# Performance work log

Measured on AMD Instinct MI355X. Metric: run time of the kernel, lower is better.

Reference implementation:

```python
import jax, jax.numpy as jnp
import numpy as np

B, S, D, H, HD = 2, 2048, 1024, 16, 64
K, L = 1024, 4  # num_codes, vq_levels


def setup_inputs() -> dict:
    key = jax.random.key(0)
    ks = jax.random.split(key, 12)
    w = lambda k, shape: jax.random.normal(k, shape, jnp.float32) * 0.02
    return {
        "x": jax.random.normal(ks[0], (B, S, D), jnp.float32),
        "ln1_g": jnp.ones((D,), jnp.float32), "ln1_b": jnp.zeros((D,), jnp.float32),
        "wq": w(ks[1], (D, D)), "wk": w(ks[2], (D, D)), "wv": w(ks[3], (D, D)),
        "wg": w(ks[4], (D, D)), "wo": w(ks[5], (D, D)),
        "ln2_g": jnp.ones((D,), jnp.float32), "ln2_b": jnp.zeros((D,), jnp.float32),
        "w1": w(ks[6], (D, 4 * D)), "b1": jnp.zeros((4 * D,), jnp.float32),
        "w2": w(ks[7], (4 * D, D)), "b2": jnp.zeros((D,), jnp.float32),
        "ln3_g": jnp.ones((D,), jnp.float32), "ln3_b": jnp.zeros((D,), jnp.float32),
        "codebooks": jax.random.uniform(ks[8], (L, K, D), jnp.float32, -1.0 / K, 1.0 / K),
    }


def _ln(x, g, b):
    m = jnp.mean(x, -1, keepdims=True)
    v = jnp.var(x, -1, keepdims=True)
    return (x - m) / jnp.sqrt(v + 1e-5) * g + b


def _rope(x):  # x: [B, S, H, HD]
    hd = x.shape[-1]
    inv = 1.0 / (10000.0 ** (jnp.arange(0, hd, 2, dtype=jnp.float32) / hd))
    t = jnp.arange(x.shape[1], dtype=jnp.float32)
    f = jnp.einsum('i,j->ij', t, inv)               # [S, HD/2]
    emb = jnp.concatenate([f, f], -1)               # [S, HD]
    cos = jnp.cos(emb)[None, :, None, :]
    sin = jnp.sin(emb)[None, :, None, :]
    x1, x2 = jnp.split(x, 2, -1)
    rot = jnp.concatenate([-x2, x1], -1)
    return x * cos + rot * sin


def reference(x, ln1_g, ln1_b, wq, wk, wv, wg, wo, ln2_g, ln2_b,
              w1, b1, w2, b2, ln3_g, ln3_b, codebooks):
    # --- retention sub-block (pre-LN) ---
    h = _ln(x, ln1_g, ln1_b)
    q = (h @ wq).reshape(B, S, H, HD)
    k = (h @ wk).reshape(B, S, H, HD)
    v = (h @ wv).reshape(B, S, H, HD)
    q, k = _rope(q), _rope(k)
    q, k, v = (a.transpose(0, 2, 1, 3) for a in (q, k, v))  # [B,H,S,HD]
    i = jnp.arange(S)
    dmask = jnp.tril(i[:, None] - i[None, :]).astype(jnp.float32)  # [S,S], >=0
    gamma = (1.0 - jnp.exp2(-5.0 - jnp.arange(H, dtype=jnp.float32)))[:, None, None]
    decay = (gamma ** dmask) * jnp.tril(jnp.ones((S, S), jnp.float32))  # [H,S,S]
    ret = jnp.einsum('bhqd,bhkd->bhqk', q, k) / np.sqrt(HD).astype(np.float32) * decay
    o = jnp.einsum('bhqk,bhkd->bhqd', ret, v).transpose(0, 2, 1, 3).reshape(B, S, D)
    g = jax.nn.silu(h @ wg)
    x = x + (o * g) @ wo
    # --- MLP sub-block (pre-LN) ---
    h2 = _ln(x, ln2_g, ln2_b)
    x = x + (jax.nn.gelu(h2 @ w1 + b1, approximate=False) @ w2 + b2)
    # --- residual vector quantizer ---
    xn = _ln(x, ln3_g, ln3_b)
    residual, total = xn, jnp.zeros_like(xn)
    ql, el = 0.0, 0.0
    for lvl in range(L):
        cb = codebooks[lvl]                         # [K, D]
        flat = residual.reshape(-1, D)              # [B*S, D]
        d2 = (jnp.sum(flat ** 2, 1, keepdims=True)
              + jnp.sum(cb ** 2, 1) - 2.0 * flat @ cb.T)
        idx = jnp.argmin(d2, 1)
        quant = cb[idx].reshape(xn.shape)
        ql = ql + jnp.mean((quant - jax.lax.stop_gradient(residual)) ** 2)
        el = el + jnp.mean((jax.lax.stop_gradient(quant) - residual) ** 2)
        total = total + quant
        residual = residual - jax.lax.stop_gradient(quant)
    final = xn + jax.lax.stop_gradient(total - xn)  # straight-through
    return (x + final, ql / L, el / L)
```

## Files before the change

kernel.cpp:

```cpp
#include <hip/hip_runtime.h>
#include <cstdint>
#include <cstddef>

#define DEV __device__ __forceinline__

typedef __attribute__((ext_vector_type(8))) short bf16x8;
typedef __attribute__((ext_vector_type(4))) float f32x4;

typedef const __attribute__((address_space(1))) void gl_void;
typedef __attribute__((address_space(3))) void lds_void;

DEV unsigned short f2bf(float f){
  union { float f; uint32_t u; } v; v.f = f;
  uint32_t r = v.u + 0x7FFFu + ((v.u >> 16) & 1u);
  return (unsigned short)(r >> 16);
}
DEV float bf2f(unsigned short u){
  union { uint32_t u; float f; } v; v.u = ((uint32_t)u) << 16; return v.f;
}
DEV uint32_t packbf2(float a, float b){
  return (uint32_t)f2bf(a) | ((uint32_t)f2bf(b) << 16);
}

__global__ void ln_kernel(const float* __restrict__ x, const float* __restrict__ gw,
                          const float* __restrict__ bw, unsigned short* __restrict__ obf,
                          float* __restrict__ of32)
{
  const int row = blockIdx.x, t = threadIdx.x;
  const float4 v = ((const float4*)(x + (size_t)row*1024))[t];
  float s  = v.x + v.y + v.z + v.w;
  float s2 = v.x*v.x + v.y*v.y + v.z*v.z + v.w*v.w;
  #pragma unroll
  for (int o = 32; o >= 1; o >>= 1){ s += __shfl_down(s, o); s2 += __shfl_down(s2, o); }
  __shared__ float red[8];
  const int w = t >> 6, ln = t & 63;
  if (ln == 0){ red[w] = s; red[4+w] = s2; }
  __syncthreads();
  const float fs  = red[0]+red[1]+red[2]+red[3];
  const float fs2 = red[4]+red[5]+red[6]+red[7];
  const float mean = fs * (1.0f/1024.0f);
  const float var  = fs2 * (1.0f/1024.0f) - mean*mean;
  const float rstd = rsqrtf(var + 1e-5f);
  const float4 gv = ((const float4*)gw)[t];
  const float4 bv = ((const float4*)bw)[t];
  float4 o4;
  o4.x = (v.x-mean)*rstd*gv.x + bv.x;
  o4.y = (v.y-mean)*rstd*gv.y + bv.y;
  o4.z = (v.z-mean)*rstd*gv.z + bv.z;
  o4.w = (v.w-mean)*rstd*gv.w + bv.w;
  if (of32) ((float4*)(of32 + (size_t)row*1024))[t] = o4;
  ushort4 ob; ob.x = f2bf(o4.x); ob.y = f2bf(o4.y); ob.z = f2bf(o4.z); ob.w = f2bf(o4.w);
  ((ushort4*)(obf + (size_t)row*1024))[t] = ob;
}

struct Ptr5 { const float* p[5]; };
__global__ void transpose_cvt5(Ptr5 in, unsigned short* __restrict__ out)
{
  __shared__ float tile[32][33];
  const float* src = in.p[blockIdx.z];
  unsigned short* dst = out + (size_t)blockIdx.z*1048576;
  const int c0 = blockIdx.x*32, r0 = blockIdx.y*32;
  const int tx = threadIdx.x & 31, ty = threadIdx.x >> 5;
  #pragma unroll
  for (int i = 0; i < 32; i += 8)
    tile[ty+i][tx] = src[(size_t)(r0+ty+i)*1024 + c0 + tx];
  __syncthreads();
  #pragma unroll
  for (int i = 0; i < 32; i += 8)
    dst[(size_t)(c0+ty+i)*1024 + r0 + tx] = f2bf(tile[tx][ty+i]);
}

__global__ void transpose_cvt(const float* __restrict__ in, unsigned short* __restrict__ out,
                              int R, int C)
{
  __shared__ float tile[32][33];
  const int c0 = blockIdx.x*32, r0 = blockIdx.y*32;
  const int tx = threadIdx.x & 31, ty = threadIdx.x >> 5;
  #pragma unroll
  for (int i = 0; i < 32; i += 8)
    tile[ty+i][tx] = in[(size_t)(r0+ty+i)*C + c0 + tx];
  __syncthreads();
  #pragma unroll
  for (int i = 0; i < 32; i += 8)
    out[(size_t)(c0+ty+i)*R + r0 + tx] = f2bf(tile[tx][ty+i]);
}

__global__ void cvt_bf16x4(const float* __restrict__ in, unsigned short* __restrict__ out)
{
  const int i = blockIdx.x*256 + threadIdx.x;
  const float4 v = ((const float4*)in)[i];
  ushort4 o; o.x = f2bf(v.x); o.y = f2bf(v.y); o.z = f2bf(v.z); o.w = f2bf(v.w);
  ((ushort4*)out)[i] = o;
}

__global__ void cbn2_kernel(const float* __restrict__ cb, float* __restrict__ cbn2)
{
  const int w = threadIdx.x >> 6, ln = threadIdx.x & 63;
  const int code = blockIdx.x*4 + w;
  const float4* cr = (const float4*)(cb + (size_t)code*1024);
  float s = 0.f;
  for (int i = ln; i < 256; i += 64){ float4 v = cr[i]; s += v.x*v.x+v.y*v.y+v.z*v.z+v.w*v.w; }
  #pragma unroll
  for (int o = 32; o >= 1; o >>= 1) s += __shfl_down(s, o);
  if (ln == 0) cbn2[code] = s;
}

__global__ void rope_kernel(unsigned short* __restrict__ q, unsigned short* __restrict__ k)
{
  const int tid = blockIdx.x*256 + threadIdx.x;
  const int j  = tid & 31;
  const int hh = (tid >> 5) & 15;
  const int s_ = (tid >> 9) & 2047;
  const int b  = tid >> 20;
  const float inv = exp2f(-(float)j * 0.4152410118609203f);
  const float f = (float)s_ * inv;
  float sn, cs; sincosf(f, &sn, &cs);
  const size_t base = ((size_t)(b*2048 + s_))*1024 + hh*64 + j;
  {
    float x1 = bf2f(q[base]), x2 = bf2f(q[base+32]);
    q[base]    = f2bf(x1*cs - x2*sn);
    q[base+32] = f2bf(x2*cs + x1*sn);
  }
  {
    float x1 = bf2f(k[base]), x2 = bf2f(k[base+32]);
    k[base]    = f2bf(x1*cs - x2*sn);
    k[base+32] = f2bf(x2*cs + x1*sn);
  }
}

template<int EPI, bool BIAS, bool RES, bool OUTBF>
__global__ __launch_bounds__(256, 2) void gemm_bt(
    const unsigned short* __restrict__ A, const unsigned short* __restrict__ BT,
    void* __restrict__ Cv, const float* __restrict__ bias, const float* __restrict__ resid,
    int M, int N, int K)
{
  __shared__ __align__(16) unsigned short As[2][128*64];
  __shared__ __align__(16) unsigned short Bs[2][128*64];
  const int t = threadIdx.x;
  const int w = t >> 6, ln = t & 63, lg = ln >> 4, lc = ln & 15;
  const int gx = gridDim.x, nwg = gridDim.x * gridDim.y;
  int lin = blockIdx.y * gx + blockIdx.x;
  lin = (lin >> 3) + (lin & 7) * (nwg >> 3);
  const int m0 = (lin / gx) * 128, n0 = (lin % gx) * 128;
  const int wr = (w >> 1) * 64, wc = (w & 1) * 64;
  f32x4 acc[4][4] = {};
  const int nkt = K >> 6;

  auto stage = [&](int buf, int kt){
    #pragma unroll
    for (int c = 0; c < 4; ++c){
      const int chunk = c*256 + t;
      const int row = chunk >> 3;
      const int kb = (((chunk & 7) << 4) ^ ((row & 7) << 4)) >> 1;
      __builtin_amdgcn_global_load_lds(
          (gl_void*)(A + (size_t)(m0+row)*K + (size_t)kt*64 + kb),
          (lds_void*)&As[buf][(c*256 + w*64)*8], 16, 0, 0);
      __builtin_amdgcn_global_load_lds(
          (gl_void*)(BT + (size_t)(n0+row)*K + (size_t)kt*64 + kb),
          (lds_void*)&Bs[buf][(c*256 + w*64)*8], 16, 0, 0);
    }
  };

  stage(0, 0);
  __syncthreads();
  for (int kt = 0; kt < nkt; ++kt){
    const int cur = kt & 1;
    if (kt + 1 < nkt) stage(cur ^ 1, kt + 1);
    #pragma unroll
    for (int ks = 0; ks < 2; ++ks){
      bf16x8 af[4], bfr[4];
      #pragma unroll
      for (int i = 0; i < 4; ++i){
        const int rowA = wr + i*16 + lc;
        const int rowB = wc + i*16 + lc;
        const int colA = (((ks<<6) + (lg<<4)) ^ ((rowA & 7) << 4)) >> 1;
        const int colB = (((ks<<6) + (lg<<4)) ^ ((rowB & 7) << 4)) >> 1;
        af[i]  = *(const bf16x8*)&As[cur][rowA*64 + colA];
        bfr[i] = *(const bf16x8*)&Bs[cur][rowB*64 + colB];
      }
      #pragma unroll
      for (int m = 0; m < 4; ++m)
        #pragma unroll
        for (int n = 0; n < 4; ++n)
          acc[m][n] = __builtin_amdgcn_mfma_f32_16x16x32_bf16(af[m], bfr[n], acc[m][n], 0, 0, 0);
    }
    __syncthreads();
  }

  #pragma unroll
  for (int m = 0; m < 4; ++m){
    #pragma unroll
    for (int n = 0; n < 4; ++n){
      #pragma unroll
      for (int r = 0; r < 4; ++r){
        const int row = m0 + wr + m*16 + lg*4 + r;
        const int col = n0 + wc + n*16 + lc;
        float v = acc[m][n][r];
        if constexpr (BIAS) v += bias[col];
        if constexpr (EPI == 1) v = v * (1.0f / (1.0f + __expf(-v)));
        if constexpr (EPI == 2) v = 0.5f * v * (1.0f + erff(v * 0.70710678118654752f));
        if constexpr (EPI == 3){
          const int sect = col >> 10;
          float ov = v;
          if (sect == 3) ov = v * (1.0f / (1.0f + __expf(-v)));
          ((unsigned short*)Cv)[(size_t)sect*4194304 + (size_t)row*1024 + (col & 1023)] = f2bf(ov);
          continue;
        }
        if constexpr (RES) v += resid[(size_t)row*N + col];
        if constexpr (OUTBF) ((unsigned short*)Cv)[(size_t)row*N + col] = f2bf(v);
        else                 ((float*)Cv)[(size_t)row*N + col] = v;
      }
    }
  }
}

template<int EPI, bool BIAS, bool RES, bool OUTBF, int NSPLIT>
__global__ __launch_bounds__(256, 3) void gemm64_bt(
    const unsigned short* __restrict__ A, const unsigned short* __restrict__ BT,
    void* __restrict__ Cv, const float* __restrict__ bias, const float* __restrict__ resid,
    int M, int N, int K)
{
  __shared__ __align__(16) unsigned short As[2][64*64];
  __shared__ __align__(16) unsigned short Bs[2][128*64];
  const int t = threadIdx.x;
  const int w = t >> 6, ln = t & 63, lg = ln >> 4, lc = ln & 15;
  const int gx = gridDim.x, nwg = gridDim.x * gridDim.y;
  int lin = blockIdx.y * gx + blockIdx.x;
  lin = (lin >> 3) + (lin & 7) * (nwg >> 3);
  const int bx = lin % gx, by = lin / gx;
  const int m0 = by * 64, n0 = bx * 128;
  const int wr = (w >> 1) * 32, wc = (w & 1) * 64;
  f32x4 acc[2][4] = {};
  const int nkt = (K >> 6) / NSPLIT;
  const int ktb = (NSPLIT > 1) ? blockIdx.z * nkt : 0;

  auto stage = [&](int buf, int kt){
    {
      const int chunk = t;
    }
    #pragma unroll
    for (int c = 0; c < 2; ++c){
      const int chunk = c*256 + t;
      const int row = chunk >> 3;
      const int kb = (((chunk & 7) << 4) ^ ((row & 7) << 4)) >> 1;
      __builtin_amdgcn_global_load_lds(
          (gl_void*)(A + (size_t)(m0+row)*K + (size_t)(ktb+kt)*64 + kb),
          (lds_void*)&As[buf][(c*256 + w*64)*8], 16, 0, 0);
    }
    #pragma unroll
    for (int c = 0; c < 4; ++c){
      const int chunk = c*256 + t;
      const int row = chunk >> 3;
      const int kb = (((chunk & 7) << 4) ^ ((row & 7) << 4)) >> 1;
      __builtin_amdgcn_global_load_lds(
          (gl_void*)(BT + (size_t)(n0+row)*K + (size_t)(ktb+kt)*64 + kb),
          (lds_void*)&Bs[buf][(c*256 + w*64)*8], 16, 0, 0);
    }
  };

  stage(0, 0);
  __syncthreads();
  for (int kt = 0; kt < nkt; ++kt){
    const int cur = kt & 1;
    if (kt + 1 < nkt) stage(cur ^ 1, kt + 1);
    #pragma unroll
    for (int ks = 0; ks < 2; ++ks){
      bf16x8 af[2], bfr[4];
      #pragma unroll
      for (int i = 0; i < 2; ++i){
        const int rowA = wr + i*16 + lc;
        const int colA = (((ks<<6) + (lg<<4)) ^ ((rowA & 7) << 4)) >> 1;
        af[i] = *(const bf16x8*)&As[cur][rowA*64 + colA];
      }
      #pragma unroll
      for (int i = 0; i < 4; ++i){
        const int rowB = wc + i*16 + lc;
        const int colB = (((ks<<6) + (lg<<4)) ^ ((rowB & 7) << 4)) >> 1;
        bfr[i] = *(const bf16x8*)&Bs[cur][rowB*64 + colB];
      }
      #pragma unroll
      for (int m = 0; m < 2; ++m)
        #pragma unroll
        for (int n = 0; n < 4; ++n)
          acc[m][n] = __builtin_amdgcn_mfma_f32_16x16x32_bf16(af[m], bfr[n], acc[m][n], 0, 0, 0);
    }
    __syncthreads();
  }

  if constexpr (EPI == 4){
    #pragma unroll
    for (int m = 0; m < 2; ++m){
      #pragma unroll
      for (int r = 0; r < 4; ++r){
        float best = 3.4e38f; int bi = 0;
        #pragma unroll
        for (int n = 0; n < 4; ++n){
          const int col = n0 + wc + n*16 + lc;
          const float d = bias[col] - 2.0f*acc[m][n][r];
          if (d < best){ best = d; bi = col; }
        }
        #pragma unroll
        for (int o = 1; o < 16; o <<= 1){
          const float ob = __shfl_xor(best, o);
          const int oi = __shfl_xor(bi, o);
          if (ob < best || (ob == best && oi < bi)){ best = ob; bi = oi; }
        }
        if (lc == 0){
          const int row = m0 + wr + m*16 + lg*4 + r;
          ((float2*)Cv)[row*16 + bx*2 + (w & 1)] = make_float2(best, (float)bi);
        }
      }
    }
    return;
  }

  float* Cp = (float*)Cv + (NSPLIT > 1 ? (size_t)blockIdx.z * (size_t)M * N : 0);
  #pragma unroll
  for (int m = 0; m < 2; ++m){
    #pragma unroll
    for (int n = 0; n < 4; ++n){
      #pragma unroll
      for (int r = 0; r < 4; ++r){
        const int row = m0 + wr + m*16 + lg*4 + r;
        const int col = n0 + wc + n*16 + lc;
        float v = acc[m][n][r];
        if constexpr (BIAS) v += bias[col];
        if constexpr (RES) v += resid[(size_t)row*N + col];
        if constexpr (OUTBF) ((unsigned short*)Cv)[(size_t)row*N + col] = f2bf(v);
        else                 Cp[(size_t)row*N + col] = v;
      }
    }
  }
}

__global__ void splitk_reduce(const float* __restrict__ p, const float* __restrict__ bias,
                              const float* __restrict__ resid, float* __restrict__ out)
{
  const int i = blockIdx.x*256 + threadIdx.x;
  const float4 a = ((const float4*)p)[i];
  const float4 b = ((const float4*)(p + 4194304))[i];
  const float4 rv = ((const float4*)resid)[i];
  const float4 bv = ((const float4*)bias)[i & 255];
  float4 o;
  o.x = a.x + b.x + rv.x + bv.x;
  o.y = a.y + b.y + rv.y + bv.y;
  o.z = a.z + b.z + rv.z + bv.z;
  o.w = a.w + b.w + rv.w + bv.w;
  ((float4*)out)[i] = o;
}

__global__ __launch_bounds__(256, 2) void chunk_sum(
    const unsigned short* __restrict__ kb, const unsigned short* __restrict__ vb,
    float* __restrict__ Tbuf)
{
  __shared__ unsigned short KT[64*72];
  __shared__ unsigned short VT[64*72];
  const int t = threadIdx.x, w = t >> 6, ln = t & 63, lg = ln >> 4, lc = ln & 15;
  const int blk = blockIdx.x;
  const int bh = blk >> 5, c = blk & 31;
  const int b = bh >> 4, hh = bh & 15;
  const float lg2g = log2f(1.0f - exp2f(-5.0f - (float)hh));
  #pragma unroll
  for (int ch = 0; ch < 2; ++ch){
    const int chunk = ch*256 + t;
    const int i = chunk >> 3, d0 = (chunk & 7)*8;
    const size_t gofs = ((size_t)(b*2048 + c*64 + i))*1024 + hh*64 + d0;
    const float wi = exp2f(lg2g * (float)(64 - i));
    union {uint4 u; unsigned short s[8];} kv, vv;
    kv.u = *(const uint4*)(kb + gofs);
    vv.u = *(const uint4*)(vb + gofs);
    #pragma unroll
    for (int j = 0; j < 8; ++j){
      KT[(d0+j)*72 + i] = f2bf(bf2f(kv.s[j]) * wi);
      VT[(d0+j)*72 + i] = vv.s[j];
    }
  }
  __syncthreads();
  f32x4 acc[4] = {};
  #pragma unroll
  for (int ks = 0; ks < 2; ++ks){
    const bf16x8 af = *(const bf16x8*)&KT[(w*16 + lc)*72 + ks*32 + lg*8];
    #pragma unroll
    for (int n = 0; n < 4; ++n){
      const bf16x8 bf = *(const bf16x8*)&VT[(n*16 + lc)*72 + ks*32 + lg*8];
      acc[n] = __builtin_amdgcn_mfma_f32_16x16x32_bf16(af, bf, acc[n], 0, 0, 0);
    }
  }
  float* out = Tbuf + (size_t)blk*4096;
  #pragma unroll
  for (int n = 0; n < 4; ++n)
    #pragma unroll
    for (int r = 0; r < 4; ++r)
      out[(w*16 + lg*4 + r)*64 + n*16 + lc] = acc[n][r];
}

__global__ void chunk_scan(const float* __restrict__ Tbuf, unsigned short* __restrict__ statesT)
{
  const int bh = blockIdx.x, t = threadIdx.x;
  const int hh = bh & 15;
  const float gamma = 1.0f - exp2f(-5.0f - (float)hh);
  const float g64 = exp2f(log2f(gamma) * 64.0f);
  float S[16];
  #pragma unroll
  for (int j = 0; j < 16; ++j) S[j] = 0.f;
  const int dv = t >> 2, d0 = (t & 3) * 16;
  for (int c = 0; c < 32; ++c){
    const size_t base = ((size_t)(bh*32 + c))*4096;
    union { unsigned short s[8]; uint4 u; } p0, p1;
    #pragma unroll
    for (int j = 0; j < 8; ++j){ p0.s[j] = f2bf(S[j]); p1.s[j] = f2bf(S[8+j]); }
    *(uint4*)(statesT + base + t*16)     = p0.u;
    *(uint4*)(statesT + base + t*16 + 8) = p1.u;
    #pragma unroll
    for (int j = 0; j < 16; ++j)
      S[j] = g64*S[j] + Tbuf[base + (size_t)(d0 + j)*64 + dv];
  }
}

__global__ __launch_bounds__(256, 2) void retention_chunk(
    const unsigned short* __restrict__ qb, const unsigned short* __restrict__ kb,
    const unsigned short* __restrict__ vb, const unsigned short* __restrict__ gb,
    const unsigned short* __restrict__ statesT, unsigned short* __restrict__ og)
{
  __shared__ unsigned short VT[64*72];
  __shared__ unsigned short Pw[64*72];
  const int t = threadIdx.x, w = t >> 6, ln = t & 63, lg = ln >> 4, lc = ln & 15;
  const int blk = blockIdx.x;
  const int bh = blk >> 5, c = blk & 31;
  const int b = bh >> 4, hh = bh & 15;
  const float lg2g = log2f(1.0f - exp2f(-5.0f - (float)hh));
  float gpr[4];
  #pragma unroll
  for (int r = 0; r < 4; ++r) gpr[r] = exp2f(-lg2g * (float)r);
  const size_t rowbase = (size_t)(b*2048 + c*64);

  #pragma unroll
  for (int ch = 0; ch < 2; ++ch){
    const int chunk = ch*256 + t;
    const int i = chunk >> 3, d0 = (chunk & 7)*8;
    union {uint4 u; unsigned short s[8];} vv;
    vv.u = *(const uint4*)(vb + (rowbase + i)*1024 + hh*64 + d0);
    #pragma unroll
    for (int j = 0; j < 8; ++j) VT[(d0+j)*72 + i] = vv.s[j];
  }

  bf16x8 Qf[2], Kf[4][2];
  #pragma unroll
  for (int ks = 0; ks < 2; ++ks){
    union {uint4 u; bf16x8 f;} cv;
    cv.u = *(const uint4*)(qb + (rowbase + w*16 + lc)*1024 + hh*64 + ks*32 + lg*8);
    Qf[ks] = cv.f;
    #pragma unroll
    for (int mt = 0; mt < 4; ++mt){
      union {uint4 u; bf16x8 f;} kv;
      kv.u = *(const uint4*)(kb + (rowbase + mt*16 + lc)*1024 + hh*64 + ks*32 + lg*8);
      Kf[mt][ks] = kv.f;
    }
  }

  f32x4 st[4] = {};
  #pragma unroll
  for (int ks = 0; ks < 2; ++ks)
    #pragma unroll
    for (int mt = 0; mt < 4; ++mt)
      st[mt] = __builtin_amdgcn_mfma_f32_16x16x32_bf16(Kf[mt][ks], Qf[ks], st[mt], 0, 0, 0);

  __syncthreads();

  #pragma unroll
  for (int mt = 0; mt < 4; ++mt){
    const int kp = mt*16 + lg*4;
    const int qrow = w*16 + lc;
    const int delta0 = qrow - kp;
    const float dec0 = exp2f(lg2g * (float)delta0) * 0.125f;
    float vals[4];
    #pragma unroll
    for (int r = 0; r < 4; ++r)
      vals[r] = (delta0 >= r) ? st[mt][r] * dec0 * gpr[r] : 0.0f;
    uint2 pk; pk.x = packbf2(vals[0], vals[1]); pk.y = packbf2(vals[2], vals[3]);
    *(uint2*)&Pw[qrow*72 + kp] = pk;
  }

  f32x4 acc[4] = {};
  const unsigned short* Sbase = statesT + (size_t)blk*4096;
  #pragma unroll
  for (int ks = 0; ks < 2; ++ks)
    #pragma unroll
    for (int n = 0; n < 4; ++n){
      union {uint4 u; bf16x8 f;} sv;
      sv.u = *(const uint4*)(Sbase + (n*16 + lc)*64 + ks*32 + lg*8);
      acc[n] = __builtin_amdgcn_mfma_f32_16x16x32_bf16(Qf[ks], sv.f, acc[n], 0, 0, 0);
    }
  #pragma unroll
  for (int n = 0; n < 4; ++n)
    #pragma unroll
    for (int r = 0; r < 4; ++r)
      acc[n][r] *= exp2f(lg2g * (float)(w*16 + lg*4 + r)) * 0.125f;

  #pragma unroll
  for (int ks = 0; ks < 2; ++ks){
    const bf16x8 Pf = *(const bf16x8*)&Pw[(w*16 + lc)*72 + ks*32 + lg*8];
    #pragma unroll
    for (int n = 0; n < 4; ++n){
      const bf16x8 Vf = *(const bf16x8*)&VT[(n*16 + lc)*72 + ks*32 + lg*8];
      acc[n] = __builtin_amdgcn_mfma_f32_16x16x32_bf16(Pf, Vf, acc[n], 0, 0, 0);
    }
  }

  #pragma unroll
  for (int n = 0; n < 4; ++n){
    #pragma unroll
    for (int r = 0; r < 4; ++r){
      const size_t row = rowbase + w*16 + lg*4 + r;
      const int col = hh*64 + n*16 + lc;
      const float gv = bf2f(gb[row*1024 + col]);
      og[row*1024 + col] = f2bf(acc[n][r] * gv);
    }
  }
}

__global__ void rvq_update2(const float* __restrict__ cb_l, const float2* __restrict__ partials,
                            float* __restrict__ res, unsigned short* __restrict__ resb,
                            float* __restrict__ total, float* __restrict__ qlpart, int lvl)
{
  const int m = blockIdx.x, t = threadIdx.x;
  __shared__ int sid;
  if (t == 0){
    float best = 3.4e38f; int bi = 0;
    #pragma unroll
    for (int p = 0; p < 16; ++p){
      const float2 pr = partials[m*16 + p];
      if (pr.x < best){ best = pr.x; bi = (int)pr.y; }
    }
    sid = bi;
  }
  __syncthreads();
  const int id = sid;
  const float4 qv = ((const float4*)(cb_l + (size_t)id*1024))[t];
  const float4 rv = ((const float4*)(res + (size_t)m*1024))[t];
  float4 nr; nr.x = rv.x - qv.x; nr.y = rv.y - qv.y; nr.z = rv.z - qv.z; nr.w = rv.w - qv.w;
  float4 tv;
  if (lvl == 0){ tv = qv; }
  else { tv = ((const float4*)(total + (size_t)m*1024))[t];
         tv.x += qv.x; tv.y += qv.y; tv.z += qv.z; tv.w += qv.w; }
  ((float4*)(total + (size_t)m*1024))[t] = tv;
  ((float4*)(res   + (size_t)m*1024))[t] = nr;
  ushort4 nb; nb.x = f2bf(nr.x); nb.y = f2bf(nr.y); nb.z = f2bf(nr.z); nb.w = f2bf(nr.w);
  ((ushort4*)(resb + (size_t)m*1024))[t] = nb;
  float s = nr.x*nr.x + nr.y*nr.y + nr.z*nr.z + nr.w*nr.w;
  #pragma unroll
  for (int o = 32; o >= 1; o >>= 1) s += __shfl_down(s, o);
  __shared__ float red[4];
  if ((t & 63) == 0) red[t >> 6] = s;
  __syncthreads();
  if (t == 0) qlpart[lvl*4096 + m] = red[0]+red[1]+red[2]+red[3];
}

__global__ void final_add(const float* __restrict__ x2, const float* __restrict__ total,
                          float* __restrict__ out)
{
  int i = blockIdx.x*256 + threadIdx.x;
  const float4* a = (const float4*)x2;
  const float4* b = (const float4*)total;
  float4* o = (float4*)out;
  for (; i < 4194304/4; i += gridDim.x*256){
    float4 va = a[i], vb = b[i];
    va.x += vb.x; va.y += vb.y; va.z += vb.z; va.w += vb.w;
    o[i] = va;
  }
}

__global__ void ql_final(const float* __restrict__ qlpart, float* __restrict__ outs)
{
  const int t = threadIdx.x;
  float s = 0.f;
  for (int i = t; i < 16384; i += 256) s += qlpart[i];
  #pragma unroll
  for (int o = 32; o >= 1; o >>= 1) s += __shfl_down(s, o);
  __shared__ float red[4];
  if ((t & 63) == 0) red[t >> 6] = s;
  __syncthreads();
  if (t == 0){
    const float q = (red[0]+red[1]+red[2]+red[3]) * (1.0f/4194304.0f) * 0.25f;
    outs[0] = q; outs[1] = q;
  }
}

extern "C" void kernel_launch(void* const* d_in, const int* in_sizes, int n_in,
                              void* d_out, int out_size, void* d_ws, size_t ws_size,
                              hipStream_t stream)
{
  const float* x     = (const float*)d_in[0];
  const float* ln1_g = (const float*)d_in[1];
  const float* ln1_b = (const float*)d_in[2];
  const float* wq    = (const float*)d_in[3];
  const float* wk    = (const float*)d_in[4];
  const float* wv    = (const float*)d_in[5];
  const float* wg    = (const float*)d_in[6];
  const float* wo    = (const float*)d_in[7];
  const float* ln2_g = (const float*)d_in[8];
  const float* ln2_b = (const float*)d_in[9];
  const float* w1    = (const float*)d_in[10];
  const float* b1    = (const float*)d_in[11];
  const float* w2    = (const float*)d_in[12];
  const float* b2    = (const float*)d_in[13];
  const float* ln3_g = (const float*)d_in[14];
  const float* ln3_b = (const float*)d_in[15];
  const float* cb    = (const float*)d_in[16];

  char* ws = (char*)d_ws;
  const size_t MB = 1024*1024;
  unsigned short* wqkvgT = (unsigned short*)(ws + 0*MB);
  unsigned short* woT  = (unsigned short*)(ws + 8*MB);
  unsigned short* w1T  = (unsigned short*)(ws + 10*MB);
  unsigned short* w2T  = (unsigned short*)(ws + 18*MB);
  unsigned short* cbbf = (unsigned short*)(ws + 26*MB);
  float* cbn2     = (float*)(ws + 34*MB);
  float* qlpart   = (float*)(ws + 34*MB + 16*1024);
  float2* partials= (float2*)(ws + 34*MB + 128*1024);
  unsigned short* hbf  = (unsigned short*)(ws + 35*MB);
  unsigned short* qbuf = (unsigned short*)(ws + 43*MB);
  unsigned short* kbuf = (unsigned short*)(ws + 51*MB);
  unsigned short* vbuf = (unsigned short*)(ws + 59*MB);
  unsigned short* gbuf = (unsigned short*)(ws + 67*MB);
  float* skbuf  = (float*)(ws + 43*MB);
  unsigned short* ogb  = (unsigned short*)(ws + 75*MB);
  float* x1     = (float*)(ws + 83*MB);
  unsigned short* h2   = (unsigned short*)(ws + 99*MB);
  unsigned short* a1   = (unsigned short*)(ws + 107*MB);
  float* x2     = (float*)(ws + 139*MB);
  float* Tbuf   = (float*)(ws + 139*MB);
  float* resf   = (float*)(ws + 155*MB);
  unsigned short* statesT = (unsigned short*)(ws + 155*MB);
  unsigned short* resb = (unsigned short*)(ws + 171*MB);
  float* totalb = (float*)(ws + 187*MB);

  float* outf = (float*)d_out;

  Ptr5 p5; p5.p[0]=wq; p5.p[1]=wk; p5.p[2]=wv; p5.p[3]=wg; p5.p[4]=wo;
  hipLaunchKernelGGL(transpose_cvt5, dim3(32,32,5), dim3(256), 0, stream, p5, wqkvgT);
  hipLaunchKernelGGL(transpose_cvt, dim3(128,32), dim3(256), 0, stream, w1, w1T, 1024, 4096);
  hipLaunchKernelGGL(transpose_cvt, dim3(32,128), dim3(256), 0, stream, w2, w2T, 4096, 1024);
  hipLaunchKernelGGL(cvt_bf16x4,    dim3(4096),   dim3(256), 0, stream, cb, cbbf);
  hipLaunchKernelGGL(cbn2_kernel,   dim3(1024),   dim3(256), 0, stream, cb, cbn2);

  hipLaunchKernelGGL(ln_kernel, dim3(4096), dim3(256), 0, stream, x, ln1_g, ln1_b, hbf, (float*)nullptr);
  hipLaunchKernelGGL((gemm_bt<3,false,false,true>), dim3(32,32), dim3(256), 0, stream,
                     hbf, wqkvgT, (void*)qbuf, (const float*)nullptr, (const float*)nullptr, 4096, 4096, 1024);
  hipLaunchKernelGGL(rope_kernel, dim3(8192), dim3(256), 0, stream, qbuf, kbuf);
  hipLaunchKernelGGL(chunk_sum,  dim3(1024), dim3(256), 0, stream, kbuf, vbuf, Tbuf);
  hipLaunchKernelGGL(chunk_scan, dim3(32),   dim3(256), 0, stream, Tbuf, statesT);
  hipLaunchKernelGGL(retention_chunk, dim3(1024), dim3(256), 0, stream,
                     qbuf, kbuf, vbuf, gbuf, statesT, ogb);
  hipLaunchKernelGGL((gemm64_bt<0,false,true,false,1>), dim3(8,64), dim3(256), 0, stream,
                     ogb, wqkvgT + 4194304, (void*)x1, (const float*)nullptr, x, 4096, 1024, 1024);

  hipLaunchKernelGGL(ln_kernel, dim3(4096), dim3(256), 0, stream, x1, ln2_g, ln2_b, h2, (float*)nullptr);
  hipLaunchKernelGGL((gemm_bt<2,true,false,true>), dim3(32,32), dim3(256), 0, stream,
                     h2, w1T, (void*)a1, b1, (const float*)nullptr, 4096, 4096, 1024);
  hipLaunchKernelGGL((gemm64_bt<0,false,false,false,2>), dim3(8,64,2), dim3(256), 0, stream,
                     a1, w2T, (void*)skbuf, (const float*)nullptr, (const float*)nullptr, 4096, 1024, 4096);
  hipLaunchKernelGGL(splitk_reduce, dim3(4096), dim3(256), 0, stream, skbuf, b2, x1, x2);

  hipLaunchKernelGGL(ln_kernel, dim3(4096), dim3(256), 0, stream, x2, ln3_g, ln3_b, resb, resf);
  for (int lvl = 0; lvl < 4; ++lvl){
    hipLaunchKernelGGL((gemm64_bt<4,false,false,false,1>), dim3(8,64), dim3(256), 0, stream,
                       resb, cbbf + (size_t)lvl*1048576, (void*)partials,
                       cbn2 + lvl*1024, (const float*)nullptr, 4096, 1024, 1024);
    hipLaunchKernelGGL(rvq_update2, dim3(4096), dim3(256), 0, stream,
                       cb + (size_t)lvl*1048576, partials, resf, resb,
                       totalb, qlpart, lvl);
  }

  hipLaunchKernelGGL(final_add, dim3(2048), dim3(256), 0, stream, x2, totalb, outf);
  hipLaunchKernelGGL(ql_final, dim3(1), dim3(256), 0, stream, qlpart, outf + 4194304);
}
```

Baseline: 443.6 us.

## Fuse RoPE into QKV GEMM epilogue, merge codebook prep, drop RVQ total buffer

RoPE now runs in the QKV/G GEMM epilogue, pairing accumulator tiles n and n^2, and the standalone rope kernel is removed. The codebook bf16 conversion and norm computation are merged into one kernel. The RVQ total accumulator is replaced by the identity total = xn - final residual, which removes per-level total reads and writes. gemm_bt is also retiled to a K-step of 32 with an unswizzled LDS layout and launch bounds raised to 4 waves per SIMD, trading possible LDS bank conflicts and more barriers for higher occupancy.

Measured after the change: 433.0 us. -2.4%, faster.

```diff
diff --git a/kernel.cpp b/kernel.cpp
--- a/kernel.cpp
+++ b/kernel.cpp
@@ -85,57 +85,30 @@
     out[(size_t)(c0+ty+i)*R + r0 + tx] = f2bf(tile[tx][ty+i]);
 }
 
-__global__ void cvt_bf16x4(const float* __restrict__ in, unsigned short* __restrict__ out)
-{
-  const int i = blockIdx.x*256 + threadIdx.x;
-  const float4 v = ((const float4*)in)[i];
+__global__ void cvtnorm_kernel(const float* __restrict__ cb, unsigned short* __restrict__ cbbf,
+                               float* __restrict__ cbn2)
+{
+  const int code = blockIdx.x, t = threadIdx.x;
+  const float4 v = ((const float4*)(cb + (size_t)code*1024))[t];
   ushort4 o; o.x = f2bf(v.x); o.y = f2bf(v.y); o.z = f2bf(v.z); o.w = f2bf(v.w);
-  ((ushort4*)out)[i] = o;
-}
-
-__global__ void cbn2_kernel(const float* __restrict__ cb, float* __restrict__ cbn2)
-{
-  const int w = threadIdx.x >> 6, ln = threadIdx.x & 63;
-  const int code = blockIdx.x*4 + w;
-  const float4* cr = (const float4*)(cb + (size_t)code*1024);
-  float s = 0.f;
-  for (int i = ln; i < 256; i += 64){ float4 v = cr[i]; s += v.x*v.x+v.y*v.y+v.z*v.z+v.w*v.w; }
-  #pragma unroll
-  for (int o = 32; o >= 1; o >>= 1) s += __shfl_down(s, o);
-  if (ln == 0) cbn2[code] = s;
-}
-
-__global__ void rope_kernel(unsigned short* __restrict__ q, unsigned short* __restrict__ k)
-{
-  const int tid = blockIdx.x*256 + threadIdx.x;
-  const int j  = tid & 31;
-  const int hh = (tid >> 5) & 15;
-  const int s_ = (tid >> 9) & 2047;
-  const int b  = tid >> 20;
-  const float inv = exp2f(-(float)j * 0.4152410118609203f);
-  const float f = (float)s_ * inv;
-  float sn, cs; sincosf(f, &sn, &cs);
-  const size_t base = ((size_t)(b*2048 + s_))*1024 + hh*64 + j;
-  {
-    float x1 = bf2f(q[base]), x2 = bf2f(q[base+32]);
-    q[base]    = f2bf(x1*cs - x2*sn);
-    q[base+32] = f2bf(x2*cs + x1*sn);
-  }
-  {
-    float x1 = bf2f(k[base]), x2 = bf2f(k[base+32]);
-    k[base]    = f2bf(x1*cs - x2*sn);
-    k[base+32] = f2bf(x2*cs + x1*sn);
-  }
+  ((ushort4*)(cbbf + (size_t)code*1024))[t] = o;
+  float s = v.x*v.x + v.y*v.y + v.z*v.z + v.w*v.w;
+  #pragma unroll
+  for (int off = 32; off >= 1; off >>= 1) s += __shfl_down(s, off);
+  __shared__ float red[4];
+  if ((t & 63) == 0) red[t >> 6] = s;
+  __syncthreads();
+  if (t == 0) cbn2[code] = red[0]+red[1]+red[2]+red[3];
 }
 
 template<int EPI, bool BIAS, bool RES, bool OUTBF>
-__global__ __launch_bounds__(256, 2) void gemm_bt(
+__global__ __launch_bounds__(256, 4) void gemm_bt(
     const unsigned short* __restrict__ A, const unsigned short* __restrict__ BT,
     void* __restrict__ Cv, const float* __restrict__ bias, const float* __restrict__ resid,
     int M, int N, int K)
 {
-  __shared__ __align__(16) unsigned short As[2][128*64];
-  __shared__ __align__(16) unsigned short Bs[2][128*64];
+  __shared__ __align__(16) unsigned short As[2][128*32];
+  __shared__ __align__(16) unsigned short Bs[2][128*32];
   const int t = threadIdx.x;
   const int w = t >> 6, ln = t & 63, lg = ln >> 4, lc = ln & 15;
   const int gx = gridDim.x, nwg = gridDim.x * gridDim.y;
@@ -144,19 +117,18 @@
   const int m0 = (lin / gx) * 128, n0 = (lin % gx) * 128;
   const int wr = (w >> 1) * 64, wc = (w & 1) * 64;
   f32x4 acc[4][4] = {};
-  const int nkt = K >> 6;
+  const int nkt = K >> 5;
 
   auto stage = [&](int buf, int kt){
     #pragma unroll
-    for (int c = 0; c < 4; ++c){
+    for (int c = 0; c < 2; ++c){
       const int chunk = c*256 + t;
-      const int row = chunk >> 3;
-      const int kb = (((chunk & 7) << 4) ^ ((row & 7) << 4)) >> 1;
+      const int row = chunk >> 2, ke = (chunk & 3) * 8;
       __builtin_amdgcn_global_load_lds(
-          (gl_void*)(A + (size_t)(m0+row)*K + (size_t)kt*64 + kb),
+          (gl_void*)(A + (size_t)(m0+row)*K + (size_t)kt*32 + ke),
           (lds_void*)&As[buf][(c*256 + w*64)*8], 16, 0, 0);
       __builtin_amdgcn_global_load_lds(
-          (gl_void*)(BT + (size_t)(n0+row)*K + (size_t)kt*64 + kb),
+          (gl_void*)(BT + (size_t)(n0+row)*K + (size_t)kt*32 + ke),
           (lds_void*)&Bs[buf][(c*256 + w*64)*8], 16, 0, 0);
     }
   };
@@ -166,25 +138,48 @@
   for (int kt = 0; kt < nkt; ++kt){
     const int cur = kt & 1;
     if (kt + 1 < nkt) stage(cur ^ 1, kt + 1);
-    #pragma unroll
-    for (int ks = 0; ks < 2; ++ks){
-      bf16x8 af[4], bfr[4];
-      #pragma unroll
-      for (int i = 0; i < 4; ++i){
-        const int rowA = wr + i*16 + lc;
-        const int rowB = wc + i*16 + lc;
-        const int colA = (((ks<<6) + (lg<<4)) ^ ((rowA & 7) << 4)) >> 1;
-        const int colB = (((ks<<6) + (lg<<4)) ^ ((rowB & 7) << 4)) >> 1;
-        af[i]  = *(const bf16x8*)&As[cur][rowA*64 + colA];
-        bfr[i] = *(const bf16x8*)&Bs[cur][rowB*64 + colB];
+    bf16x8 af[4], bfr[4];
+    #pragma unroll
+    for (int i = 0; i < 4; ++i){
+      af[i]  = *(const bf16x8*)&As[cur][(wr + i*16 + lc)*32 + lg*8];
+      bfr[i] = *(const bf16x8*)&Bs[cur][(wc + i*16 + lc)*32 + lg*8];
+    }
+    #pragma unroll
+    for (int m = 0; m < 4; ++m)
+      #pragma unroll
+      for (int n = 0; n < 4; ++n)
+        acc[m][n] = __builtin_amdgcn_mfma_f32_16x16x32_bf16(af[m], bfr[n], acc[m][n], 0, 0, 0);
+    __syncthreads();
+  }
+
+  if constexpr (EPI == 3){
+    const int sect = (n0 + wc) >> 10;
+    unsigned short* outp = (unsigned short*)Cv + (size_t)sect*4194304;
+    #pragma unroll
+    for (int m = 0; m < 4; ++m){
+      #pragma unroll
+      for (int r = 0; r < 4; ++r){
+        const int row = m0 + wr + m*16 + lg*4 + r;
+        const int s_ = row & 2047;
+        #pragma unroll
+        for (int n = 0; n < 4; ++n){
+          const int col = n0 + wc + n*16 + lc;
+          const int c1 = col & 1023;
+          float v = acc[m][n][r];
+          if (sect <= 1){
+            const int j = c1 & 31;
+            const float ang = (float)s_ * exp2f(-(float)j * 0.4152410118609203f);
+            float sn, cs; sincosf(ang, &sn, &cs);
+            const float vp = acc[m][n ^ 2][r];
+            v = (c1 & 32) ? (v*cs + vp*sn) : (v*cs - vp*sn);
+          } else if (sect == 3){
+            v = v * (1.0f / (1.0f + __expf(-v)));
+          }
+          outp[(size_t)row*1024 + c1] = f2bf(v);
+        }
       }
-      #pragma unroll
-      for (int m = 0; m < 4; ++m)
-        #pragma unroll
-        for (int n = 0; n < 4; ++n)
-          acc[m][n] = __builtin_amdgcn_mfma_f32_16x16x32_bf16(af[m], bfr[n], acc[m][n], 0, 0, 0);
-    }
-    __syncthreads();
+    }
+    return;
   }
 
   #pragma unroll
@@ -199,13 +194,6 @@
         if constexpr (BIAS) v += bias[col];
         if constexpr (EPI == 1) v = v * (1.0f / (1.0f + __expf(-v)));
         if constexpr (EPI == 2) v = 0.5f * v * (1.0f + erff(v * 0.70710678118654752f));
-        if constexpr (EPI == 3){
-          const int sect = col >> 10;
-          float ov = v;
-          if (sect == 3) ov = v * (1.0f / (1.0f + __expf(-v)));
-          ((unsigned short*)Cv)[(size_t)sect*4194304 + (size_t)row*1024 + (col & 1023)] = f2bf(ov);
-          continue;
-        }
         if constexpr (RES) v += resid[(size_t)row*N + col];
         if constexpr (OUTBF) ((unsigned short*)Cv)[(size_t)row*N + col] = f2bf(v);
         else                 ((float*)Cv)[(size_t)row*N + col] = v;
@@ -235,9 +223,6 @@
   const int ktb = (NSPLIT > 1) ? blockIdx.z * nkt : 0;
 
   auto stage = [&](int buf, int kt){
-    {
-      const int chunk = t;
-    }
     #pragma unroll
     for (int c = 0; c < 2; ++c){
       const int chunk = c*256 + t;
@@ -519,9 +504,9 @@
   }
 }
 
-__global__ void rvq_update2(const float* __restrict__ cb_l, const float2* __restrict__ partials,
-                            float* __restrict__ res, unsigned short* __restrict__ resb,
-                            float* __restrict__ total, float* __restrict__ qlpart, int lvl)
+__global__ void rvq_update3(const float* __restrict__ cb_l, const float2* __restrict__ partials,
+                            const float* __restrict__ res_in, float* __restrict__ res_out,
+                            unsigned short* __restrict__ resb, float* __restrict__ qlpart, int lvl)
 {
   const int m = blockIdx.x, t = threadIdx.x;
   __shared__ int sid;
@@ -537,14 +522,9 @@
   __syncthreads();
   const int id = sid;
   const float4 qv = ((const float4*)(cb_l + (size_t)id*1024))[t];
-  const float4 rv = ((const float4*)(res + (size_t)m*1024))[t];
+  const float4 rv = ((const float4*)(res_in + (size_t)m*1024))[t];
   float4 nr; nr.x = rv.x - qv.x; nr.y = rv.y - qv.y; nr.z = rv.z - qv.z; nr.w = rv.w - qv.w;
-  float4 tv;
-  if (lvl == 0){ tv = qv; }
-  else { tv = ((const float4*)(total + (size_t)m*1024))[t];
-         tv.x += qv.x; tv.y += qv.y; tv.z += qv.z; tv.w += qv.w; }
-  ((float4*)(total + (size_t)m*1024))[t] = tv;
-  ((float4*)(res   + (size_t)m*1024))[t] = nr;
+  ((float4*)(res_out + (size_t)m*1024))[t] = nr;
   ushort4 nb; nb.x = f2bf(nr.x); nb.y = f2bf(nr.y); nb.z = f2bf(nr.z); nb.w = f2bf(nr.w);
   ((ushort4*)(resb + (size_t)m*1024))[t] = nb;
   float s = nr.x*nr.x + nr.y*nr.y + nr.z*nr.z + nr.w*nr.w;
@@ -556,18 +536,19 @@
   if (t == 0) qlpart[lvl*4096 + m] = red[0]+red[1]+red[2]+red[3];
 }
 
-__global__ void final_add(const float* __restrict__ x2, const float* __restrict__ total,
-                          float* __restrict__ out)
-{
-  int i = blockIdx.x*256 + threadIdx.x;
-  const float4* a = (const float4*)x2;
-  const float4* b = (const float4*)total;
-  float4* o = (float4*)out;
-  for (; i < 4194304/4; i += gridDim.x*256){
-    float4 va = a[i], vb = b[i];
-    va.x += vb.x; va.y += vb.y; va.z += vb.z; va.w += vb.w;
-    o[i] = va;
-  }
+__global__ void final_add3(const float* __restrict__ x2, const float* __restrict__ xn,
+                           const float* __restrict__ res4, float* __restrict__ out)
+{
+  const int i = blockIdx.x*256 + threadIdx.x;
+  const float4 a = ((const float4*)x2)[i];
+  const float4 b = ((const float4*)xn)[i];
+  const float4 c = ((const float4*)res4)[i];
+  float4 o;
+  o.x = a.x + b.x - c.x;
+  o.y = a.y + b.y - c.y;
+  o.z = a.z + b.z - c.z;
+  o.w = a.w + b.w - c.w;
+  ((float4*)out)[i] = o;
 }
 
 __global__ void ql_final(const float* __restrict__ qlpart, float* __restrict__ outs)
@@ -611,7 +592,6 @@
   char* ws = (char*)d_ws;
   const size_t MB = 1024*1024;
   unsigned short* wqkvgT = (unsigned short*)(ws + 0*MB);
-  unsigned short* woT  = (unsigned short*)(ws + 8*MB);
   unsigned short* w1T  = (unsigned short*)(ws + 10*MB);
   unsigned short* w2T  = (unsigned short*)(ws + 18*MB);
   unsigned short* cbbf = (unsigned short*)(ws + 26*MB);
@@ -630,10 +610,10 @@
   unsigned short* a1   = (unsigned short*)(ws + 107*MB);
   float* x2     = (float*)(ws + 139*MB);
   float* Tbuf   = (float*)(ws + 139*MB);
-  float* resf   = (float*)(ws + 155*MB);
+  float* xnf    = (float*)(ws + 155*MB);
   unsigned short* statesT = (unsigned short*)(ws + 155*MB);
   unsigned short* resb = (unsigned short*)(ws + 171*MB);
-  float* totalb = (float*)(ws + 187*MB);
+  float* resw   = (float*)(ws + 187*MB);
 
   float* outf = (float*)d_out;
 
@@ -641,13 +621,11 @@
   hipLaunchKernelGGL(transpose_cvt5, dim3(32,32,5), dim3(256), 0, stream, p5, wqkvgT);
   hipLaunchKernelGGL(transpose_cvt, dim3(128,32), dim3(256), 0, stream, w1, w1T, 1024, 4096);
   hipLaunchKernelGGL(transpose_cvt, dim3(32,128), dim3(256), 0, stream, w2, w2T, 4096, 1024);
-  hipLaunchKernelGGL(cvt_bf16x4,    dim3(4096),   dim3(256), 0, stream, cb, cbbf);
-  hipLaunchKernelGGL(cbn2_kernel,   dim3(1024),   dim3(256), 0, stream, cb, cbn2);
+  hipLaunchKernelGGL(cvtnorm_kernel, dim3(4096), dim3(256), 0, stream, cb, cbbf, cbn2);
 
   hipLaunchKernelGGL(ln_kernel, dim3(4096), dim3(256), 0, stream, x, ln1_g, ln1_b, hbf, (float*)nullptr);
   hipLaunchKernelGGL((gemm_bt<3,false,false,true>), dim3(32,32), dim3(256), 0, stream,
                      hbf, wqkvgT, (void*)qbuf, (const float*)nullptr, (const float*)nullptr, 4096, 4096, 1024);
-  hipLaunchKernelGGL(rope_kernel, dim3(8192), dim3(256), 0, stream, qbuf, kbuf);
   hipLaunchKernelGGL(chunk_sum,  dim3(1024), dim3(256), 0, stream, kbuf, vbuf, Tbuf);
   hipLaunchKernelGGL(chunk_scan, dim3(32),   dim3(256), 0, stream, Tbuf, statesT);
   hipLaunchKernelGGL(retention_chunk, dim3(1024), dim3(256), 0, stream,
@@ -662,16 +640,16 @@
                      a1, w2T, (void*)skbuf, (const float*)nullptr, (const float*)nullptr, 4096, 1024, 4096);
   hipLaunchKernelGGL(splitk_reduce, dim3(4096), dim3(256), 0, stream, skbuf, b2, x1, x2);
 
-  hipLaunchKernelGGL(ln_kernel, dim3(4096), dim3(256), 0, stream, x2, ln3_g, ln3_b, resb, resf);
+  hipLaunchKernelGGL(ln_kernel, dim3(4096), dim3(256), 0, stream, x2, ln3_g, ln3_b, resb, xnf);
   for (int lvl = 0; lvl < 4; ++lvl){
     hipLaunchKernelGGL((gemm64_bt<4,false,false,false,1>), dim3(8,64), dim3(256), 0, stream,
                        resb, cbbf + (size_t)lvl*1048576, (void*)partials,
                        cbn2 + lvl*1024, (const float*)nullptr, 4096, 1024, 1024);
-    hipLaunchKernelGGL(rvq_update2, dim3(4096), dim3(256), 0, stream,
-                       cb + (size_t)lvl*1048576, partials, resf, resb,
-                       totalb, qlpart, lvl);
-  }
-
-  hipLaunchKernelGGL(final_add, dim3(2048), dim3(256), 0, stream, x2, totalb, outf);
+    hipLaunchKernelGGL(rvq_update3, dim3(4096), dim3(256), 0, stream,
+                       cb + (size_t)lvl*1048576, partials,
+                       (lvl == 0) ? xnf : resw, resw, resb, qlpart, lvl);
+  }
+
+  hipLaunchKernelGGL(final_add3, dim3(4096), dim3(256), 0, stream, x2, xnf, resw, outf);
   hipLaunchKernelGGL(ql_final, dim3(1), dim3(256), 0, stream, qlpart, outf + 4194304);
 }
```
